# Optimization experiments

Measured on AMD Instinct MI355X. Metric: run time of the kernel, lower is better.

Reference implementation:

```python
import jax, jax.numpy as jnp
import numpy as np

T, B, D, NQ = 1024, 4096, 16, 4  # seq_len, batch, input_dim, n_qubits (= hidden_dim)


def _qlayer(angles, phi):
    """Simulate: RX(angles) encode + trainable RX(phi) per wire + CNOT chain + PauliZ expvals.
    Since the initial state is |0..0> and all single-qubit gates are RX (which compose as
    RX(a)RX(b)=RX(a+b)), the pre-entanglement state is a product state with per-wire
    probabilities p1 = sin^2((a+phi)/2); CNOTs permute basis states, hence permute probs.
    Returns <Z_w> per wire, shape [B, n]."""
    Bsz, n = angles.shape
    theta = angles + phi[None, :]
    p1 = jnp.sin(0.5 * theta) ** 2  # [B, n]
    probs = jnp.ones((Bsz, 1), angles.dtype)
    for w in range(n):  # outer product over wires -> [B, 2^n], wire 0 = most significant
        pw = jnp.stack([1.0 - p1[:, w], p1[:, w]], axis=-1)  # [B, 2]
        probs = (probs[:, :, None] * pw[:, None, :]).reshape(Bsz, -1)
    psi = probs.reshape((Bsz,) + (2,) * n)
    for c in range(n - 1):  # CNOT(c, c+1): flip target amplitudes where control = 1
        ax = c + 1
        s0 = jnp.take(psi, 0, axis=ax)
        s1 = jnp.flip(jnp.take(psi, 1, axis=ax), axis=ax)  # target axis after removal = ax
        psi = jnp.stack([s0, s1], axis=ax)
    probs = psi.reshape(Bsz, -1)
    bits = (jnp.arange(2 ** n)[None, :] >> (n - 1 - jnp.arange(n))[:, None]) & 1  # [n, 2^n]
    signs = (1 - 2 * bits).astype(angles.dtype)
    return probs @ signs.T  # [B, n]


def setup_inputs() -> dict:
    key = jax.random.key(0)
    ks = jax.random.split(key, 16)
    H = NQ  # hidden_dim == n_qubits structurally
    s = 0.1
    inp = {
        "inputs": jax.random.normal(ks[0], (T, B, D), dtype=jnp.float32),
        "W_f": jax.random.normal(ks[1], (NQ, D + H), dtype=jnp.float32) * s,
        "b_f": jax.random.normal(ks[2], (NQ,), dtype=jnp.float32) * s,
        "W_i": jax.random.normal(ks[3], (NQ, D + H), dtype=jnp.float32) * s,
        "b_i": jax.random.normal(ks[4], (NQ,), dtype=jnp.float32) * s,
        "W_g": jax.random.normal(ks[5], (NQ, D + H), dtype=jnp.float32) * s,
        "b_g": jax.random.normal(ks[6], (NQ,), dtype=jnp.float32) * s,
        "W_o": jax.random.normal(ks[7], (NQ, D + H), dtype=jnp.float32) * s,
        "b_o": jax.random.normal(ks[8], (NQ,), dtype=jnp.float32) * s,
        "rx_f": jax.random.normal(ks[9], (NQ,), dtype=jnp.float32),
        "rx_i": jax.random.normal(ks[10], (NQ,), dtype=jnp.float32),
        "rx_g": jax.random.normal(ks[11], (NQ,), dtype=jnp.float32),
        "rx_o": jax.random.normal(ks[12], (NQ,), dtype=jnp.float32),
    }
    return inp


def reference(inputs, W_f, b_f, W_i, b_i, W_g, b_g, W_o, b_o, rx_f, rx_i, rx_g, rx_o):
    Tn, Bn, Dn = inputs.shape
    H = rx_f.shape[0]
    hx = jnp.zeros((Bn, H), inputs.dtype)
    cx = jnp.zeros((Bn, H), inputs.dtype)

    def step(carry, x):
        hx, cx = carry
        comb = jnp.concatenate([x, hx], axis=1)  # [B, D+H]
        f = jax.nn.sigmoid(_qlayer(comb @ W_f.T + b_f, rx_f))
        i = jax.nn.sigmoid(_qlayer(comb @ W_i.T + b_i, rx_i))
        g = jnp.tanh(_qlayer(comb @ W_g.T + b_g, rx_g))
        o = jax.nn.sigmoid(_qlayer(comb @ W_o.T + b_o, rx_o))
        cx2 = f * cx + i * g
        hx2 = o * jnp.tanh(cx2)
        return (hx2, cx2), hx2

    (hx, cx), stacked = jax.lax.scan(step, (hx, cx), inputs)
    return stacked, hx, cx
```

## Files before the change

### kernel.cpp

```cpp
#include <hip/hip_runtime.h>

#define T_LEN 1024
#define B_SZ  4096

#define DPP_QP(a,b,c,d) ((a)|((b)<<2)|((c)<<4)|((d)<<6))
#define DPP_QPX1 DPP_QP(1,0,3,2)
#define DPP_QPX2 DPP_QP(2,3,0,1)
#define DPP_QPX3 DPP_QP(3,2,1,0)
#define DPP_BCAST0 DPP_QP(0,0,0,0)
#define DPP_BCAST1 DPP_QP(1,1,1,1)
#define DPP_BCAST2 DPP_QP(2,2,2,2)
#define DPP_BCAST3 DPP_QP(3,3,3,3)
#define DPP_ROW_SHR(n) (0x110|(n))
#define DPP_ROW_ROR(n) (0x120|(n))

template <int CTRL>
__device__ __forceinline__ float dppf(float x) {
  return __int_as_float(__builtin_amdgcn_update_dpp(
      0, __float_as_int(x), CTRL, 0xF, 0xF, true));
}
template <int CTRL>
__device__ __forceinline__ float dppf_id1(float x) {
  return __int_as_float(__builtin_amdgcn_update_dpp(
      0x3f800000, __float_as_int(x), CTRL, 0xF, 0xF, false));
}

__global__ void __launch_bounds__(64, 1) qlstm_65481071402744_kernel(
    const float* __restrict__ x,
    const float* __restrict__ Wf, const float* __restrict__ bfv,
    const float* __restrict__ Wi, const float* __restrict__ biv,
    const float* __restrict__ Wg, const float* __restrict__ bgv,
    const float* __restrict__ Wo, const float* __restrict__ bov,
    const float* __restrict__ rxf, const float* __restrict__ rxi,
    const float* __restrict__ rxg, const float* __restrict__ rxo,
    float* __restrict__ out) {
  const int tid = threadIdx.x;
  const int g = tid & 3;
  const int w = (tid >> 2) & 3;
  const int b = (blockIdx.x << 2) + (tid >> 4);

  auto Wsel = [&](int gg) -> const float* {
    return gg == 0 ? Wf : gg == 1 ? Wi : gg == 2 ? Wg : Wo;
  };

  float Wxp[4][4];
#pragma unroll
  for (int j = 0; j < 4; ++j) {
    const float* Wt = Wsel(g ^ j);
#pragma unroll
    for (int d = 0; d < 4; ++d) Wxp[j][d] = Wt[w * 20 + (g << 2) + d];
  }
  const float* Wown = Wsel(g);
  float Whp[4];
#pragma unroll
  for (int k = 0; k < 4; ++k) Whp[k] = Wown[w * 20 + 16 + ((w + k) & 3)];

  const float* bown = g == 0 ? bfv : g == 1 ? biv : g == 2 ? bgv : bov;
  const float* rxown = g == 0 ? rxf : g == 1 ? rxi : g == 2 ? rxg : rxo;
  const float zinit = bown[w] + rxown[w];

  constexpr float L2E = 1.4426950408889634f;
  const bool isG = (g == 2);
  const float nlscale = isG ? -2.0f * L2E : -L2E;
  const float nla = isG ? 2.0f : 1.0f;
  const float nlb = isG ? -1.0f : 0.0f;

  float hx = 0.0f, cx = 0.0f;

  const float4* xp4 = (const float4*)x + ((size_t)b << 2) + g;
  float4 xr[8];
#pragma unroll
  for (int u = 0; u < 8; ++u) xr[u] = xp4[(size_t)u * (B_SZ * 4)];

  float* outp = out + ((size_t)b << 2) + w;

  for (int tb = 0; tb < T_LEN / 8; ++tb) {
    float hb[8];
#pragma unroll
    for (int u = 0; u < 8; ++u) {
      const int t = (tb << 3) + u;
      const float4 xq = xr[u];
      int tl = t + 8;
      tl = tl < T_LEN ? tl : T_LEN - 1;
      xr[u] = xp4[(size_t)tl * (B_SZ * 4)];

      float p0 = fmaf(Wxp[0][0], xq.x, zinit);
      p0 = fmaf(Wxp[0][1], xq.y, p0);
      p0 = fmaf(Wxp[0][2], xq.z, p0);
      p0 = fmaf(Wxp[0][3], xq.w, p0);
      float p1 = fmaf(Wxp[1][3], xq.w, fmaf(Wxp[1][2], xq.z, fmaf(Wxp[1][1], xq.y, Wxp[1][0] * xq.x)));
      float p2 = fmaf(Wxp[2][3], xq.w, fmaf(Wxp[2][2], xq.z, fmaf(Wxp[2][1], xq.y, Wxp[2][0] * xq.x)));
      float p3 = fmaf(Wxp[3][3], xq.w, fmaf(Wxp[3][2], xq.z, fmaf(Wxp[3][1], xq.y, Wxp[3][0] * xq.x)));

      const float zx = (p0 + dppf<DPP_QPX1>(p1)) +
                       (dppf<DPP_QPX2>(p2) + dppf<DPP_QPX3>(p3));

      const float h1 = dppf<DPP_ROW_ROR(12)>(hx);
      const float h2 = dppf<DPP_ROW_ROR(8)>(hx);
      const float h3 = dppf<DPP_ROW_ROR(4)>(hx);
      float za = fmaf(Whp[0], hx, zx);
      za = fmaf(Whp[1], h1, za);
      const float zb = fmaf(Whp[3], h3, Whp[2] * h2);
      const float z = za + zb;

      const float c = __builtin_amdgcn_cosf(
          __builtin_amdgcn_fractf(z * 0.15915494309189535f));

      float q = c * dppf_id1<DPP_ROW_SHR(4)>(c);
      q = q * dppf_id1<DPP_ROW_SHR(8)>(q);

      const float ee = __builtin_amdgcn_exp2f(q * nlscale);
      const float s = fmaf(__builtin_amdgcn_rcpf(1.0f + ee), nla, nlb);

      const float fA = dppf<DPP_BCAST0>(s);
      const float iA = dppf<DPP_BCAST1>(s);
      const float gA = dppf<DPP_BCAST2>(s);
      const float oA = dppf<DPP_BCAST3>(s);

      cx = fmaf(fA, cx, iA * gA);
      const float e3 = __builtin_amdgcn_exp2f(cx * (-2.0f * L2E));
      const float th = fmaf(2.0f, __builtin_amdgcn_rcpf(1.0f + e3), -1.0f);
      hx = oA * th;
      hb[u] = hx;
    }
    if (g == 0) {
#pragma unroll
      for (int u = 0; u < 8; ++u)
        outp[(size_t)((tb << 3) + u) * (B_SZ * 4)] = hb[u];
    }
  }

  if (g == 0) {
    const size_t base = (size_t)T_LEN * B_SZ * 4;
    out[base + (b << 2) + w] = hx;
    out[base + B_SZ * 4 + (b << 2) + w] = cx;
  }
}

extern "C" void kernel_launch(void* const* d_in, const int* in_sizes, int n_in,
                              void* d_out, int out_size, void* d_ws, size_t ws_size,
                              hipStream_t stream) {
  const float* x   = (const float*)d_in[0];
  const float* Wf  = (const float*)d_in[1];
  const float* bf_ = (const float*)d_in[2];
  const float* Wi  = (const float*)d_in[3];
  const float* bi_ = (const float*)d_in[4];
  const float* Wg  = (const float*)d_in[5];
  const float* bg_ = (const float*)d_in[6];
  const float* Wo  = (const float*)d_in[7];
  const float* bo_ = (const float*)d_in[8];
  const float* rxf = (const float*)d_in[9];
  const float* rxi = (const float*)d_in[10];
  const float* rxg = (const float*)d_in[11];
  const float* rxo = (const float*)d_in[12];

  qlstm_65481071402744_kernel<<<(B_SZ * 16) / 64, 64, 0, stream>>>(
      x, Wf, bf_, Wi, bi_, Wg, bg_, Wo, bo_, rxf, rxi, rxg, rxo,
      (float*)d_out);
}
```

Measured before the change: 519.9 us.

## Split input projection and recurrence into producer/consumer waves via LDS double buffer

Each block now has two waves. One wave computes the input projection W_x·x + bias for 32-step chunks and writes it, pre-scaled by 1/(2π) and wrapped with fract, into a double-buffered LDS array. The other wave reads those values and runs only the serial hidden-state recurrence, so the x loads and projection arithmetic leave the per-step dependency chain. The fract and scaling are also moved out of the recurrence by folding 1/(2π) into the weights. In exchange it adds a block barrier per chunk, LDS traffic, and twice the waves per block, which may compete with the recurrence wave for SIMD issue slots.

New measurement: 430.5 us. 17.2% less time.

```diff
diff --git a/kernel.cpp b/kernel.cpp
--- a/kernel.cpp
+++ b/kernel.cpp
@@ -2,6 +2,8 @@
 
 #define T_LEN 1024
 #define B_SZ  4096
+#define CHUNK 32
+#define NCHUNK (T_LEN / CHUNK)
 
 #define DPP_QP(a,b,c,d) ((a)|((b)<<2)|((c)<<4)|((d)<<6))
 #define DPP_QPX1 DPP_QP(1,0,3,2)
@@ -25,7 +27,7 @@
       0x3f800000, __float_as_int(x), CTRL, 0xF, 0xF, false));
 }
 
-__global__ void __launch_bounds__(64, 1) qlstm_65481071402744_kernel(
+__global__ void __launch_bounds__(128, 2) qlstm_65481071402744_kernel(
     const float* __restrict__ x,
     const float* __restrict__ Wf, const float* __restrict__ bfv,
     const float* __restrict__ Wi, const float* __restrict__ biv,
@@ -34,106 +36,139 @@
     const float* __restrict__ rxf, const float* __restrict__ rxi,
     const float* __restrict__ rxg, const float* __restrict__ rxo,
     float* __restrict__ out) {
+  __shared__ float zbuf[2][CHUNK][64];
+
   const int tid = threadIdx.x;
-  const int g = tid & 3;
-  const int w = (tid >> 2) & 3;
-  const int b = (blockIdx.x << 2) + (tid >> 4);
+  const int lane = tid & 63;
+  const int g = lane & 3;
+  const int w = (lane >> 2) & 3;
+  const int b = (blockIdx.x << 2) + (lane >> 4);
 
   auto Wsel = [&](int gg) -> const float* {
     return gg == 0 ? Wf : gg == 1 ? Wi : gg == 2 ? Wg : Wo;
   };
-
-  float Wxp[4][4];
-#pragma unroll
-  for (int j = 0; j < 4; ++j) {
-    const float* Wt = Wsel(g ^ j);
-#pragma unroll
-    for (int d = 0; d < 4; ++d) Wxp[j][d] = Wt[w * 20 + (g << 2) + d];
-  }
-  const float* Wown = Wsel(g);
-  float Whp[4];
-#pragma unroll
-  for (int k = 0; k < 4; ++k) Whp[k] = Wown[w * 20 + 16 + ((w + k) & 3)];
-
   const float* bown = g == 0 ? bfv : g == 1 ? biv : g == 2 ? bgv : bov;
   const float* rxown = g == 0 ? rxf : g == 1 ? rxi : g == 2 ? rxg : rxo;
-  const float zinit = bown[w] + rxown[w];
+  constexpr float INV2PI = 0.15915494309189535f;
 
-  constexpr float L2E = 1.4426950408889634f;
-  const bool isG = (g == 2);
-  const float nlscale = isG ? -2.0f * L2E : -L2E;
-  const float nla = isG ? 2.0f : 1.0f;
-  const float nlb = isG ? -1.0f : 0.0f;
+  if (tid >= 64) {
+    float Wxp[4][4];
+#pragma unroll
+    for (int j = 0; j < 4; ++j) {
+      const float* Wt = Wsel(g ^ j);
+#pragma unroll
+      for (int d = 0; d < 4; ++d)
+        Wxp[j][d] = Wt[w * 20 + (g << 2) + d] * INV2PI;
+    }
+    const float zinit = (bown[w] + rxown[w]) * INV2PI;
 
-  float hx = 0.0f, cx = 0.0f;
+    const float4* xp4 = (const float4*)x + ((size_t)b << 2) + g;
+    float4 xr[8];
+#pragma unroll
+    for (int u = 0; u < 8; ++u) xr[u] = xp4[(size_t)u * (B_SZ * 4)];
 
-  const float4* xp4 = (const float4*)x + ((size_t)b << 2) + g;
-  float4 xr[8];
+    for (int c = 0; c < NCHUNK; ++c) {
+      float* zb = &zbuf[c & 1][0][0];
 #pragma unroll
-  for (int u = 0; u < 8; ++u) xr[u] = xp4[(size_t)u * (B_SZ * 4)];
+      for (int qq = 0; qq < CHUNK / 8; ++qq) {
+#pragma unroll
+        for (int u = 0; u < 8; ++u) {
+          const int tloc = (qq << 3) + u;
+          const int t = c * CHUNK + tloc;
+          const float4 xq = xr[u];
+          int tl = t + 8;
+          tl = tl < T_LEN ? tl : T_LEN - 1;
+          xr[u] = xp4[(size_t)tl * (B_SZ * 4)];
 
-  float* outp = out + ((size_t)b << 2) + w;
+          float p0 = fmaf(Wxp[0][0], xq.x, zinit);
+          p0 = fmaf(Wxp[0][1], xq.y, p0);
+          p0 = fmaf(Wxp[0][2], xq.z, p0);
+          p0 = fmaf(Wxp[0][3], xq.w, p0);
+          float p1 = fmaf(Wxp[1][3], xq.w,
+                     fmaf(Wxp[1][2], xq.z,
+                     fmaf(Wxp[1][1], xq.y, Wxp[1][0] * xq.x)));
+          float p2 = fmaf(Wxp[2][3], xq.w,
+                     fmaf(Wxp[2][2], xq.z,
+                     fmaf(Wxp[2][1], xq.y, Wxp[2][0] * xq.x)));
+          float p3 = fmaf(Wxp[3][3], xq.w,
+                     fmaf(Wxp[3][2], xq.z,
+                     fmaf(Wxp[3][1], xq.y, Wxp[3][0] * xq.x)));
 
-  for (int tb = 0; tb < T_LEN / 8; ++tb) {
-    float hb[8];
+          const float zx = (p0 + dppf<DPP_QPX1>(p1)) +
+                           (dppf<DPP_QPX2>(p2) + dppf<DPP_QPX3>(p3));
+          zb[tloc * 64 + lane] = __builtin_amdgcn_fractf(zx);
+        }
+      }
+      __syncthreads();
+    }
+  } else {
+    const float* Wown = Wsel(g);
+    float Whs[4];
 #pragma unroll
-    for (int u = 0; u < 8; ++u) {
-      const int t = (tb << 3) + u;
-      const float4 xq = xr[u];
-      int tl = t + 8;
-      tl = tl < T_LEN ? tl : T_LEN - 1;
-      xr[u] = xp4[(size_t)tl * (B_SZ * 4)];
+    for (int k = 0; k < 4; ++k)
+      Whs[k] = Wown[w * 20 + 16 + ((w + k) & 3)] * INV2PI;
 
-      float p0 = fmaf(Wxp[0][0], xq.x, zinit);
-      p0 = fmaf(Wxp[0][1], xq.y, p0);
-      p0 = fmaf(Wxp[0][2], xq.z, p0);
-      p0 = fmaf(Wxp[0][3], xq.w, p0);
-      float p1 = fmaf(Wxp[1][3], xq.w, fmaf(Wxp[1][2], xq.z, fmaf(Wxp[1][1], xq.y, Wxp[1][0] * xq.x)));
-      float p2 = fmaf(Wxp[2][3], xq.w, fmaf(Wxp[2][2], xq.z, fmaf(Wxp[2][1], xq.y, Wxp[2][0] * xq.x)));
-      float p3 = fmaf(Wxp[3][3], xq.w, fmaf(Wxp[3][2], xq.z, fmaf(Wxp[3][1], xq.y, Wxp[3][0] * xq.x)));
+    constexpr float L2E = 1.4426950408889634f;
+    const bool isG = (g == 2);
+    const float nlscale = isG ? -2.0f * L2E : -L2E;
+    const float nla = isG ? 2.0f : 1.0f;
+    const float nlb = isG ? -1.0f : 0.0f;
 
-      const float zx = (p0 + dppf<DPP_QPX1>(p1)) +
-                       (dppf<DPP_QPX2>(p2) + dppf<DPP_QPX3>(p3));
+    float hx = 0.0f, cx = 0.0f;
+    float* outp = out + ((size_t)b << 2) + w;
 
-      const float h1 = dppf<DPP_ROW_ROR(12)>(hx);
-      const float h2 = dppf<DPP_ROW_ROR(8)>(hx);
-      const float h3 = dppf<DPP_ROW_ROR(4)>(hx);
-      float za = fmaf(Whp[0], hx, zx);
-      za = fmaf(Whp[1], h1, za);
-      const float zb = fmaf(Whp[3], h3, Whp[2] * h2);
-      const float z = za + zb;
+    for (int c = 0; c < NCHUNK; ++c) {
+      __syncthreads();
+      const float* zb = &zbuf[c & 1][0][0];
+#pragma unroll
+      for (int qq = 0; qq < CHUNK / 8; ++qq) {
+        float hb[8];
+#pragma unroll
+        for (int u = 0; u < 8; ++u) {
+          const int tloc = (qq << 3) + u;
+          const float zxf = zb[tloc * 64 + lane];
 
-      const float c = __builtin_amdgcn_cosf(
-          __builtin_amdgcn_fractf(z * 0.15915494309189535f));
+          const float h1 = dppf<DPP_ROW_ROR(12)>(hx);
+          const float h2 = dppf<DPP_ROW_ROR(8)>(hx);
+          const float h3 = dppf<DPP_ROW_ROR(4)>(hx);
+          float za = fmaf(Whs[0], hx, zxf);
+          za = fmaf(Whs[1], h1, za);
+          const float zb2 = fmaf(Whs[3], h3, Whs[2] * h2);
+          const float z = za + zb2;
 
-      float q = c * dppf_id1<DPP_ROW_SHR(4)>(c);
-      q = q * dppf_id1<DPP_ROW_SHR(8)>(q);
+          const float ccos = __builtin_amdgcn_cosf(z);
 
-      const float ee = __builtin_amdgcn_exp2f(q * nlscale);
-      const float s = fmaf(__builtin_amdgcn_rcpf(1.0f + ee), nla, nlb);
+          float q = ccos * dppf_id1<DPP_ROW_SHR(4)>(ccos);
+          q = q * dppf_id1<DPP_ROW_SHR(8)>(q);
 
-      const float fA = dppf<DPP_BCAST0>(s);
-      const float iA = dppf<DPP_BCAST1>(s);
-      const float gA = dppf<DPP_BCAST2>(s);
-      const float oA = dppf<DPP_BCAST3>(s);
+          const float ee = __builtin_amdgcn_exp2f(q * nlscale);
+          const float s = fmaf(__builtin_amdgcn_rcpf(1.0f + ee), nla, nlb);
 
-      cx = fmaf(fA, cx, iA * gA);
-      const float e3 = __builtin_amdgcn_exp2f(cx * (-2.0f * L2E));
-      const float th = fmaf(2.0f, __builtin_amdgcn_rcpf(1.0f + e3), -1.0f);
-      hx = oA * th;
-      hb[u] = hx;
+          const float fA = dppf<DPP_BCAST0>(s);
+          const float iA = dppf<DPP_BCAST1>(s);
+          const float gA = dppf<DPP_BCAST2>(s);
+          const float oA = dppf<DPP_BCAST3>(s);
+
+          cx = fmaf(fA, cx, iA * gA);
+          const float e3 = __builtin_amdgcn_exp2f(cx * (-2.0f * L2E));
+          const float th = fmaf(2.0f, __builtin_amdgcn_rcpf(1.0f + e3), -1.0f);
+          hx = oA * th;
+          hb[u] = hx;
+        }
+        if (g == 0) {
+          const int tbase = c * CHUNK + (qq << 3);
+#pragma unroll
+          for (int u = 0; u < 8; ++u)
+            outp[(size_t)(tbase + u) * (B_SZ * 4)] = hb[u];
+        }
+      }
     }
+
     if (g == 0) {
-#pragma unroll
-      for (int u = 0; u < 8; ++u)
-        outp[(size_t)((tb << 3) + u) * (B_SZ * 4)] = hb[u];
+      const size_t base = (size_t)T_LEN * B_SZ * 4;
+      out[base + (b << 2) + w] = hx;
+      out[base + B_SZ * 4 + (b << 2) + w] = cx;
     }
-  }
-
-  if (g == 0) {
-    const size_t base = (size_t)T_LEN * B_SZ * 4;
-    out[base + (b << 2) + w] = hx;
-    out[base + B_SZ * 4 + (b << 2) + w] = cx;
   }
 }
 
@@ -154,7 +189,7 @@
   const float* rxg = (const float*)d_in[11];
   const float* rxo = (const float*)d_in[12];
 
-  qlstm_65481071402744_kernel<<<(B_SZ * 16) / 64, 64, 0, stream>>>(
+  qlstm_65481071402744_kernel<<<B_SZ / 4, 128, 0, stream>>>(
       x, Wf, bf_, Wi, bi_, Wg, bg_, Wo, bo_, rxf, rxi, rxg, rxo,
       (float*)d_out);
 }
```
